# Optimization experiments

Hardware: AMD Instinct MI355X
Metric: run time of the kernel (lower is better)

## Reference

```python
import jax, jax.numpy as jnp
import numpy as np
from jax import lax

K = 7  # kernel_size
PAD = K // 2


def _feature_difference(t):
    # t: [B, C, H, W] -> normalized census-style local differences [B, K*K, H, W]
    intensity = t.mean(axis=1, keepdims=True)  # [B,1,H,W]
    # Equivalent to conv2d with the identity (eye) kernel in the torch module:
    # channel k gathers the neighbor at offset (k//K, k%K) with zero padding.
    patches = lax.conv_general_dilated_patches(
        intensity, filter_shape=(K, K), window_strides=(1, 1),
        padding=[(PAD, PAD), (PAD, PAD)])  # [B, K*K, H, W]
    local_diff = patches - intensity
    return local_diff / jnp.sqrt(0.81 + local_diff * local_diff)


def setup_inputs() -> dict:
    key = jax.random.key(0)
    kx, ky = jax.random.split(key)
    B, C, H, W = 8, 3, 320, 1024
    x = jax.random.uniform(kx, (B, C, H, W), dtype=jnp.float32)
    y = jax.random.uniform(ky, (B, C, H, W), dtype=jnp.float32)
    return {"x": x, "y": y}


def reference(x, y):
    diff_x = _feature_difference(x)
    diff_y = _feature_difference(y)
    diff_total = diff_x - lax.stop_gradient(diff_y)  # .detach() on y branch
    d2 = diff_total * diff_total
    dist = (d2 / (0.1 + d2)).mean(axis=1, keepdims=True)  # [B,1,H,W]
    b, c, h, w = x.shape
    # valid-region mask: ones in the interior, zeros in the PAD-wide border
    mask = jnp.zeros((b, 1, h, w), dtype=x.dtype)
    mask = mask.at[:, :, PAD:h - PAD, PAD:w - PAD].set(1.0)
    return (dist * mask).mean()
```

## Files before the change

kernel.cpp:

```cpp
#include <hip/hip_runtime.h>

typedef float f32x2 __attribute__((ext_vector_type(2)));
typedef float f32x4 __attribute__((ext_vector_type(4)));

#define PAD 3
#define HH 320
#define WW 1024
#define BB 8
#define TH 32
#define TW 64
#define HALO_H (TH + 2*PAD)
#define LDS_W  72
#define NF4    (LDS_W/4)
#define NPOS   (HALO_H * NF4)
#define RPW 4
#define NWAVES 8
#define NTHREADS (NWAVES * 64)

#define NIN ((HH - 2*PAD) * (WW - 2*PAD))
#define OUT_SCALE (1.0 / (49.0 * (double)BB * (double)HH * (double)WW))
#define C0 ((float)(48.0 * (double)BB * (double)NIN * OUT_SCALE))
#define NEG_SCALE ((float)(-0.1 * OUT_SCALE))

#define KEEP(v) asm("" : "+v"(v))

__device__ __forceinline__ f32x2 mk2(float a, float b) { f32x2 r; r.x = a; r.y = b; return r; }
__device__ __forceinline__ f32x2 sp2(float a)          { f32x2 r; r.x = a; r.y = a; return r; }
__device__ __forceinline__ f32x2 fma2(f32x2 a, f32x2 b, f32x2 c) {
    return __builtin_elementwise_fma(a, b, c);
}

template<bool INTERIOR>
__device__ __forceinline__ void pair2(f32x2 nx, f32x2 ny, f32x2 cx2, f32x2 cy2,
                                      f32x2 w2, float& acc)
{
    f32x2 dx  = nx - cx2;
    f32x2 dy  = ny - cy2;
    f32x2 dx2 = dx * dx;
    f32x2 dy2 = dy * dy;
    f32x2 ax  = dx2 + sp2(0.81f);
    f32x2 ay  = dy2 + sp2(0.81f);
    f32x2 P   = ax * ay;
    f32x2 s   = mk2(__builtin_amdgcn_rsqf(P.x), __builtin_amdgcn_rsqf(P.y));
    f32x2 A   = fma2(dx2, ay, dy2 * ax);
    f32x2 h   = dx * dy;
    f32x2 inner = fma2(s, A, h * sp2(-2.0f));
    f32x2 t2  = s * inner;
    f32x2 den = t2 + sp2(0.1f);
    float ip    = __builtin_amdgcn_rcpf(den.x * den.y);
    float cross;
    if constexpr (INTERIOR) cross = den.x + den.y;
    else                    cross = fmaf(w2.x, den.y, w2.y * den.x);
    acc = fmaf(ip, cross, acc);
}

template<bool INTERIOR>
__device__ __forceinline__ float compute_rows(
    const float (&sIx)[HALO_H][LDS_W], const float (&sIy)[HALO_H][LDS_W],
    int tile_i, int tile_j, int tx, int wv)
{
    float cO[7] = {};
    f32x2 cP0 = {}, cP1 = {}, cP2 = {}, cP3 = {};
    if constexpr (!INTERIOR) {
        const int gj = tile_j + tx;
        #pragma unroll
        for (int d = 0; d < 7; ++d) {
            int nj = gj + d - 3;
            cO[d] = (nj >= PAD && nj < WW - PAD) ? 1.0f : 0.0f;
        }
        cP0 = mk2(cO[0], cO[1]);
        cP1 = mk2(cO[2], cO[3]);
        cP2 = mk2(cO[4], cO[5]);
        cP3 = sp2(cO[6]);
    }

    const int li0 = wv * RPW;

    float wx[4][7], wy[4][7];
    #pragma unroll
    for (int r = 0; r < 3; ++r) {
        #pragma unroll
        for (int d = 0; d < 7; ++d) {
            float a = sIx[li0 + 3 + r][tx + 1 + d]; KEEP(a); wx[r][d] = a;
            float c = sIy[li0 + 3 + r][tx + 1 + d]; KEEP(c); wy[r][d] = c;
        }
    }

    float acc = 0.0f;

    #pragma unroll
    for (int iu = 0; iu < RPW; ++iu) {
        const int li = li0 + iu;
        const int gi = tile_i + li;
        const int snew = (iu + 3) & 3;
        #pragma unroll
        for (int d = 0; d < 7; ++d) {
            float a = sIx[li + 6][tx + 1 + d]; KEEP(a); wx[snew][d] = a;
            float c = sIy[li + 6][tx + 1 + d]; KEEP(c); wy[snew][d] = c;
        }

        float rin[4] = {};
        f32x2 mc2 = {};
        if constexpr (!INTERIOR) {
            #pragma unroll
            for (int di = 0; di < 4; ++di) {
                int ni = gi + di;
                rin[di] = (ni >= PAD && ni < HH - PAD) ? 1.0f : 0.0f;
            }
            mc2 = sp2(rin[0] * cO[3]);
        }

        const int s0 = iu & 3;
        const f32x2 cx2 = sp2(wx[s0][3]);
        const f32x2 cy2 = sp2(wy[s0][3]);

        pair2<INTERIOR>(mk2(wx[s0][4], wx[s0][5]), mk2(wy[s0][4], wy[s0][5]),
              cx2, cy2, INTERIOR ? sp2(0.0f) : fma2(sp2(rin[0]), cP2, mc2), acc);

        #pragma unroll
        for (int di = 1; di <= 3; ++di) {
            const int s = (iu + di) & 3;
            const f32x2 rin2 = sp2(rin[di]);
            pair2<INTERIOR>(mk2(wx[s][0], wx[s][1]), mk2(wy[s][0], wy[s][1]),
                  cx2, cy2, INTERIOR ? sp2(0.0f) : fma2(rin2, cP0, mc2), acc);
            pair2<INTERIOR>(mk2(wx[s][2], wx[s][3]), mk2(wy[s][2], wy[s][3]),
                  cx2, cy2, INTERIOR ? sp2(0.0f) : fma2(rin2, cP1, mc2), acc);
            pair2<INTERIOR>(mk2(wx[s][4], wx[s][5]), mk2(wy[s][4], wy[s][5]),
                  cx2, cy2, INTERIOR ? sp2(0.0f) : fma2(rin2, cP2, mc2), acc);
        }

        {
            const int s1 = (iu + 1) & 3;
            const int s2 = (iu + 2) & 3;
            const int s3 = (iu + 3) & 3;
            pair2<INTERIOR>(mk2(wx[s0][6], wx[s1][6]), mk2(wy[s0][6], wy[s1][6]),
                  cx2, cy2, INTERIOR ? sp2(0.0f) : fma2(mk2(rin[0], rin[1]), cP3, mc2), acc);
            pair2<INTERIOR>(mk2(wx[s2][6], wx[s3][6]), mk2(wy[s2][6], wy[s3][6]),
                  cx2, cy2, INTERIOR ? sp2(0.0f) : fma2(mk2(rin[2], rin[3]), cP3, mc2), acc);
        }
    }

    return acc;
}

__global__ __launch_bounds__(NTHREADS, 4) void ternary_loss_kernel(
    const float* __restrict__ x, const float* __restrict__ y,
    float* __restrict__ out)
{
    __shared__ __align__(16) float sIx[HALO_H][LDS_W];
    __shared__ __align__(16) float sIy[HALO_H][LDS_W];
    __shared__ float wave_sums[NWAVES];

    const int tile_j = blockIdx.x * TW;
    const int tile_i = blockIdx.y * TH;
    const int b      = blockIdx.z;
    const int tx  = threadIdx.x;
    const int wv  = threadIdx.y;
    const int tid = wv * 64 + tx;

    const size_t PLANE = (size_t)HH * WW;
    const float* xb = x + (size_t)b * 3 * PLANE;
    const float* yb = y + (size_t)b * 3 * PLANE;

    for (int p = tid; p < NPOS; p += NTHREADS) {
        int r  = p / NF4;
        int c4 = p - r * NF4;
        int gi  = tile_i - PAD + r;
        int gj0 = tile_j - 4 + 4 * c4;
        f32x4 vx = {0.0f, 0.0f, 0.0f, 0.0f};
        f32x4 vy = {0.0f, 0.0f, 0.0f, 0.0f};
        if ((unsigned)gi < (unsigned)HH && (unsigned)gj0 < (unsigned)WW) {
            const float* px = xb + (size_t)gi * WW + gj0;
            f32x4 a0 = *(const f32x4*)(px);
            f32x4 a1 = *(const f32x4*)(px + PLANE);
            f32x4 a2 = *(const f32x4*)(px + 2 * PLANE);
            vx = (a0 + a1 + a2) * (1.0f / 3.0f);
            const float* py = yb + (size_t)gi * WW + gj0;
            f32x4 b0 = *(const f32x4*)(py);
            f32x4 b1 = *(const f32x4*)(py + PLANE);
            f32x4 b2 = *(const f32x4*)(py + 2 * PLANE);
            vy = (b0 + b1 + b2) * (1.0f / 3.0f);
        }
        *(f32x4*)&sIx[r][4 * c4] = vx;
        *(f32x4*)&sIy[r][4 * c4] = vy;
    }
    __syncthreads();

    const bool interior = (tile_i >= PAD) && (tile_i + TH + PAD <= HH - PAD)
                       && (tile_j >= 2*PAD) && (tile_j + TW + PAD <= WW - PAD);

    float acc;
    if (interior) acc = 2.0f * compute_rows<true >(sIx, sIy, tile_i, tile_j, tx, wv);
    else          acc =        compute_rows<false>(sIx, sIy, tile_i, tile_j, tx, wv);

    #pragma unroll
    for (int off = 32; off > 0; off >>= 1)
        acc += __shfl_down(acc, off, 64);
    if (tx == 0) wave_sums[wv] = acc;
    __syncthreads();
    if (tid == 0) {
        float total = 0.0f;
        #pragma unroll
        for (int w = 0; w < NWAVES; ++w) total += wave_sums[w];
        total *= NEG_SCALE;
        if (blockIdx.x == 0 && blockIdx.y == 0 && blockIdx.z == 0)
            total += C0;
        atomicAdd(out, total);
    }
}

extern "C" void kernel_launch(void* const* d_in, const int* in_sizes, int n_in,
                              void* d_out, int out_size, void* d_ws, size_t ws_size,
                              hipStream_t stream) {
    const float* x = (const float*)d_in[0];
    const float* y = (const float*)d_in[1];
    float* out = (float*)d_out;

    hipMemsetAsync(out, 0, sizeof(float), stream);

    dim3 grid(WW / TW, HH / TH, BB);
    dim3 block(64, NWAVES, 1);
    ternary_loss_kernel<<<grid, block, 0, stream>>>(x, y, out);
}
```

Baseline: 115.9 us.

## Give each wave a private halo tile and drop block-wide load barrier

Each of the 4 waves now loads its own 14-row halo slab into a private region of shared memory and processes 8 rows, so the __syncthreads between the load phase and the compute phase goes away. Block size shrinks from 8 waves to 4, and the row loop becomes a non-unrolled outer loop over 4-row groups. The cost is redundant halo loading: 14 rows per 8 output rows instead of 38 per 32, so more global reads and more mean computation, plus more LDS per row of output.

```diff
diff --git a/kernel.cpp b/kernel.cpp
--- a/kernel.cpp
+++ b/kernel.cpp
@@ -9,13 +9,13 @@
 #define BB 8
 #define TH 32
 #define TW 64
-#define HALO_H (TH + 2*PAD)
 #define LDS_W  72
 #define NF4    (LDS_W/4)
-#define NPOS   (HALO_H * NF4)
-#define RPW 4
-#define NWAVES 8
-#define NTHREADS (NWAVES * 64)
+#define RPW 8
+#define NWAVES 4
+#define NTHREADS 256
+#define WROWS (RPW + 6)
+#define NPOSW (WROWS * NF4)
 
 #define NIN ((HH - 2*PAD) * (WW - 2*PAD))
 #define OUT_SCALE (1.0 / (49.0 * (double)BB * (double)HH * (double)WW))
@@ -24,15 +24,15 @@
 
 #define KEEP(v) asm("" : "+v"(v))
 
-__device__ __forceinline__ f32x2 mk2(float a, float b) { f32x2 r; r.x = a; r.y = b; return r; }
-__device__ __forceinline__ f32x2 sp2(float a)          { f32x2 r; r.x = a; r.y = a; return r; }
-__device__ __forceinline__ f32x2 fma2(f32x2 a, f32x2 b, f32x2 c) {
+static __device__ __forceinline__ f32x2 mk2(float a, float b){ f32x2 r; r.x=a; r.y=b; return r; }
+static __device__ __forceinline__ f32x2 sp2(float a){ f32x2 r; r.x=a; r.y=a; return r; }
+static __device__ __forceinline__ f32x2 fma2(f32x2 a, f32x2 b, f32x2 c){
     return __builtin_elementwise_fma(a, b, c);
 }
 
 template<bool INTERIOR>
-__device__ __forceinline__ void pair2(f32x2 nx, f32x2 ny, f32x2 cx2, f32x2 cy2,
-                                      f32x2 w2, float& acc)
+static __device__ __forceinline__ void pair2(f32x2 nx, f32x2 ny, f32x2 cx2, f32x2 cy2,
+                                             f32x2 w2, float& acc)
 {
     f32x2 dx  = nx - cx2;
     f32x2 dy  = ny - cy2;
@@ -41,13 +41,13 @@
     f32x2 ax  = dx2 + sp2(0.81f);
     f32x2 ay  = dy2 + sp2(0.81f);
     f32x2 P   = ax * ay;
-    f32x2 s   = mk2(__builtin_amdgcn_rsqf(P.x), __builtin_amdgcn_rsqf(P.y));
+    f32x2 s; s.x = __builtin_amdgcn_rsqf(P.x); s.y = __builtin_amdgcn_rsqf(P.y);
     f32x2 A   = fma2(dx2, ay, dy2 * ax);
     f32x2 h   = dx * dy;
     f32x2 inner = fma2(s, A, h * sp2(-2.0f));
     f32x2 t2  = s * inner;
     f32x2 den = t2 + sp2(0.1f);
-    float ip    = __builtin_amdgcn_rcpf(den.x * den.y);
+    float ip  = __builtin_amdgcn_rcpf(den.x * den.y);
     float cross;
     if constexpr (INTERIOR) cross = den.x + den.y;
     else                    cross = fmaf(w2.x, den.y, w2.y * den.x);
@@ -55,13 +55,14 @@
 }
 
 template<bool INTERIOR>
-__device__ __forceinline__ float compute_rows(
-    const float (&sIx)[HALO_H][LDS_W], const float (&sIy)[HALO_H][LDS_W],
-    int tile_i, int tile_j, int tx, int wv)
+static __device__ __forceinline__ float compute_rows(
+    const float (&sx)[WROWS][LDS_W], const float (&sy)[WROWS][LDS_W],
+    int tile_i, int tile_j, int tx, int li0)
 {
-    float cO[7] = {};
+    float cO3 = 0.0f;
     f32x2 cP0 = {}, cP1 = {}, cP2 = {}, cP3 = {};
     if constexpr (!INTERIOR) {
+        float cO[7];
         const int gj = tile_j + tx;
         #pragma unroll
         for (int d = 0; d < 7; ++d) {
@@ -72,71 +73,68 @@
         cP1 = mk2(cO[2], cO[3]);
         cP2 = mk2(cO[4], cO[5]);
         cP3 = sp2(cO[6]);
-    }
-
-    const int li0 = wv * RPW;
+        cO3 = cO[3];
+    }
 
     float wx[4][7], wy[4][7];
     #pragma unroll
     for (int r = 0; r < 3; ++r) {
         #pragma unroll
         for (int d = 0; d < 7; ++d) {
-            float a = sIx[li0 + 3 + r][tx + 1 + d]; KEEP(a); wx[r][d] = a;
-            float c = sIy[li0 + 3 + r][tx + 1 + d]; KEEP(c); wy[r][d] = c;
+            float a = sx[3 + r][tx + 1 + d]; KEEP(a); wx[r][d] = a;
+            float c = sy[3 + r][tx + 1 + d]; KEEP(c); wy[r][d] = c;
         }
     }
 
     float acc = 0.0f;
 
-    #pragma unroll
-    for (int iu = 0; iu < RPW; ++iu) {
-        const int li = li0 + iu;
-        const int gi = tile_i + li;
-        const int snew = (iu + 3) & 3;
+    #pragma unroll 1
+    for (int io = 0; io < RPW / 4; ++io) {
         #pragma unroll
-        for (int d = 0; d < 7; ++d) {
-            float a = sIx[li + 6][tx + 1 + d]; KEEP(a); wx[snew][d] = a;
-            float c = sIy[li + 6][tx + 1 + d]; KEEP(c); wy[snew][d] = c;
-        }
-
-        float rin[4] = {};
-        f32x2 mc2 = {};
-        if constexpr (!INTERIOR) {
+        for (int iu = 0; iu < 4; ++iu) {
+            const int lr = io * 4 + iu;
+            const int gi = tile_i + li0 + lr;
+            const int sn = (iu + 3) & 3;
             #pragma unroll
-            for (int di = 0; di < 4; ++di) {
-                int ni = gi + di;
-                rin[di] = (ni >= PAD && ni < HH - PAD) ? 1.0f : 0.0f;
+            for (int d = 0; d < 7; ++d) {
+                float a = sx[lr + 6][tx + 1 + d]; KEEP(a); wx[sn][d] = a;
+                float c = sy[lr + 6][tx + 1 + d]; KEEP(c); wy[sn][d] = c;
             }
-            mc2 = sp2(rin[0] * cO[3]);
-        }
-
-        const int s0 = iu & 3;
-        const f32x2 cx2 = sp2(wx[s0][3]);
-        const f32x2 cy2 = sp2(wy[s0][3]);
-
-        pair2<INTERIOR>(mk2(wx[s0][4], wx[s0][5]), mk2(wy[s0][4], wy[s0][5]),
-              cx2, cy2, INTERIOR ? sp2(0.0f) : fma2(sp2(rin[0]), cP2, mc2), acc);
-
-        #pragma unroll
-        for (int di = 1; di <= 3; ++di) {
-            const int s = (iu + di) & 3;
-            const f32x2 rin2 = sp2(rin[di]);
-            pair2<INTERIOR>(mk2(wx[s][0], wx[s][1]), mk2(wy[s][0], wy[s][1]),
-                  cx2, cy2, INTERIOR ? sp2(0.0f) : fma2(rin2, cP0, mc2), acc);
-            pair2<INTERIOR>(mk2(wx[s][2], wx[s][3]), mk2(wy[s][2], wy[s][3]),
-                  cx2, cy2, INTERIOR ? sp2(0.0f) : fma2(rin2, cP1, mc2), acc);
-            pair2<INTERIOR>(mk2(wx[s][4], wx[s][5]), mk2(wy[s][4], wy[s][5]),
-                  cx2, cy2, INTERIOR ? sp2(0.0f) : fma2(rin2, cP2, mc2), acc);
-        }
-
-        {
-            const int s1 = (iu + 1) & 3;
-            const int s2 = (iu + 2) & 3;
-            const int s3 = (iu + 3) & 3;
+
+            float rin[4] = {};
+            f32x2 mc2 = {};
+            if constexpr (!INTERIOR) {
+                #pragma unroll
+                for (int di = 0; di < 4; ++di) {
+                    int ni = gi + di;
+                    rin[di] = (ni >= PAD && ni < HH - PAD) ? 1.0f : 0.0f;
+                }
+                mc2 = sp2(rin[0] * cO3);
+            }
+
+            const int s0 = iu & 3, s1 = (iu+1)&3, s2 = (iu+2)&3, s3_ = (iu+3)&3;
+            const f32x2 cx2 = sp2(wx[s0][3]);
+            const f32x2 cy2 = sp2(wy[s0][3]);
+
+            pair2<INTERIOR>(mk2(wx[s0][4], wx[s0][5]), mk2(wy[s0][4], wy[s0][5]),
+                cx2, cy2, INTERIOR ? sp2(0.0f) : fma2(sp2(rin[0]), cP2, mc2), acc);
+
+            #pragma unroll
+            for (int di = 1; di <= 3; ++di) {
+                const int s = (iu + di) & 3;
+                const f32x2 rin2 = sp2(rin[di]);
+                pair2<INTERIOR>(mk2(wx[s][0], wx[s][1]), mk2(wy[s][0], wy[s][1]),
+                    cx2, cy2, INTERIOR ? sp2(0.0f) : fma2(rin2, cP0, mc2), acc);
+                pair2<INTERIOR>(mk2(wx[s][2], wx[s][3]), mk2(wy[s][2], wy[s][3]),
+                    cx2, cy2, INTERIOR ? sp2(0.0f) : fma2(rin2, cP1, mc2), acc);
+                pair2<INTERIOR>(mk2(wx[s][4], wx[s][5]), mk2(wy[s][4], wy[s][5]),
+                    cx2, cy2, INTERIOR ? sp2(0.0f) : fma2(rin2, cP2, mc2), acc);
+            }
+
             pair2<INTERIOR>(mk2(wx[s0][6], wx[s1][6]), mk2(wy[s0][6], wy[s1][6]),
-                  cx2, cy2, INTERIOR ? sp2(0.0f) : fma2(mk2(rin[0], rin[1]), cP3, mc2), acc);
-            pair2<INTERIOR>(mk2(wx[s2][6], wx[s3][6]), mk2(wy[s2][6], wy[s3][6]),
-                  cx2, cy2, INTERIOR ? sp2(0.0f) : fma2(mk2(rin[2], rin[3]), cP3, mc2), acc);
+                cx2, cy2, INTERIOR ? sp2(0.0f) : fma2(mk2(rin[0], rin[1]), cP3, mc2), acc);
+            pair2<INTERIOR>(mk2(wx[s2][6], wx[s3_][6]), mk2(wy[s2][6], wy[s3_][6]),
+                cx2, cy2, INTERIOR ? sp2(0.0f) : fma2(mk2(rin[2], rin[3]), cP3, mc2), acc);
         }
     }
 
@@ -147,8 +145,8 @@
     const float* __restrict__ x, const float* __restrict__ y,
     float* __restrict__ out)
 {
-    __shared__ __align__(16) float sIx[HALO_H][LDS_W];
-    __shared__ __align__(16) float sIy[HALO_H][LDS_W];
+    __shared__ __align__(16) float sIx[NWAVES][WROWS][LDS_W];
+    __shared__ __align__(16) float sIy[NWAVES][WROWS][LDS_W];
     __shared__ float wave_sums[NWAVES];
 
     const int tile_j = blockIdx.x * TW;
@@ -162,10 +160,12 @@
     const float* xb = x + (size_t)b * 3 * PLANE;
     const float* yb = y + (size_t)b * 3 * PLANE;
 
-    for (int p = tid; p < NPOS; p += NTHREADS) {
+    const int li0 = wv * RPW;
+
+    for (int p = tx; p < NPOSW; p += 64) {
         int r  = p / NF4;
         int c4 = p - r * NF4;
-        int gi  = tile_i - PAD + r;
+        int gi  = tile_i + li0 - 3 + r;
         int gj0 = tile_j - 4 + 4 * c4;
         f32x4 vx = {0.0f, 0.0f, 0.0f, 0.0f};
         f32x4 vy = {0.0f, 0.0f, 0.0f, 0.0f};
@@ -181,17 +181,18 @@
             f32x4 b2 = *(const f32x4*)(py + 2 * PLANE);
             vy = (b0 + b1 + b2) * (1.0f / 3.0f);
         }
-        *(f32x4*)&sIx[r][4 * c4] = vx;
-        *(f32x4*)&sIy[r][4 * c4] = vy;
-    }
-    __syncthreads();
+        *(f32x4*)&sIx[wv][r][4 * c4] = vx;
+        *(f32x4*)&sIy[wv][r][4 * c4] = vy;
+    }
 
     const bool interior = (tile_i >= PAD) && (tile_i + TH + PAD <= HH - PAD)
                        && (tile_j >= 2*PAD) && (tile_j + TW + PAD <= WW - PAD);
 
     float acc;
-    if (interior) acc = 2.0f * compute_rows<true >(sIx, sIy, tile_i, tile_j, tx, wv);
-    else          acc =        compute_rows<false>(sIx, sIy, tile_i, tile_j, tx, wv);
+    if (interior)
+        acc = 2.0f * compute_rows<true >(sIx[wv], sIy[wv], tile_i, tile_j, tx, li0);
+    else
+        acc =        compute_rows<false>(sIx[wv], sIy[wv], tile_i, tile_j, tx, li0);
 
     #pragma unroll
     for (int off = 32; off > 0; off >>= 1)
@@ -199,10 +200,7 @@
     if (tx == 0) wave_sums[wv] = acc;
     __syncthreads();
     if (tid == 0) {
-        float total = 0.0f;
-        #pragma unroll
-        for (int w = 0; w < NWAVES; ++w) total += wave_sums[w];
-        total *= NEG_SCALE;
+        float total = (wave_sums[0] + wave_sums[1] + wave_sums[2] + wave_sums[3]) * NEG_SCALE;
         if (blockIdx.x == 0 && blockIdx.y == 0 && blockIdx.z == 0)
             total += C0;
         atomicAdd(out, total);
```

After: 119.3 us. 1.03x slower.
